# Kernel tuning notes

Measured on AMD Instinct MI355X. Metric: run time of the kernel, lower is better.

The kernel has to match this reference:

```python
import jax, jax.numpy as jnp
import numpy as np

N, B, FIN, FOUT = 4096, 16, 128, 128
DENSITY = 0.01


def setup_inputs() -> dict:
    key = jax.random.key(0)
    k1, k2, k3, k4 = jax.random.split(key, 4)
    # sparse binary adjacency (static pattern), stored dense for the reference
    adj = (jax.random.uniform(k1, (N, N)) < DENSITY).astype(jnp.float32)
    x = jax.random.normal(k2, (B, N, FIN), dtype=jnp.float32)
    W = jax.random.normal(k3, (FOUT, FIN), dtype=jnp.float32) * (1.0 / np.sqrt(FIN))
    b = jax.random.normal(k4, (FOUT,), dtype=jnp.float32) * 0.01
    return {"adj": adj, "x": x, "W": W, "b": b}


def _normalized_adj(adj):
    # A_hat = D^{-1/2} (A + I) D^{-1/2}, degrees from column sums (dim=0 in torch)
    a_self = adj + jnp.eye(adj.shape[0], dtype=adj.dtype)
    dinv = jax.lax.rsqrt(jnp.sum(a_self, axis=0))
    return dinv[:, None] * a_self * dinv[None, :]


def reference(adj, x, W, b):
    a_norm = _normalized_adj(adj)
    # SpMM aggregation over nodes: (N,N) x (B,N,F) -> (B,N,F)
    agg = jnp.einsum('nm,bmf->bnf', a_norm, x)
    # dense linear transform: fc(agg)
    return jnp.einsum('bnf,of->bno', agg, W) + b
```

## Files before the change

kernel.cpp:

```cpp
#include <hip/hip_runtime.h>


#define NN 4096
#define FD 128
#define NB 16
#define CAP 96
#define CPAD 104
#define XB 512

typedef float     f32x4 __attribute__((ext_vector_type(4)));
typedef _Float16  f16x4 __attribute__((ext_vector_type(4)));
typedef _Float16  f16x8 __attribute__((ext_vector_type(8)));
typedef int       i32x2 __attribute__((ext_vector_type(2)));

#define XP 136

__global__ __launch_bounds__(256) void k_bx(const float* __restrict__ A,
                                            float* __restrict__ deg,
                                            int* __restrict__ cnt,
                                            unsigned short* __restrict__ csr,
                                            const float* __restrict__ x,
                                            const float* __restrict__ W,
                                            _Float16* __restrict__ y) {
    __shared__ __align__(16) char smem[FD * XP * 2];
    const int t = threadIdx.x;

    if (blockIdx.x < XB) {
        _Float16 (*sW)[XP] = (_Float16(*)[XP])smem;
        const size_t rbase = (size_t)blockIdx.x * 128;

        #pragma unroll
        for (int i = 0; i < 8; ++i) {
            const int id = t + i * 256;
            const int o = id >> 4, f8 = (id & 15) * 8;
            const f32x4 a = *(const f32x4*)&W[(size_t)o * FD + f8];
            const f32x4 b = *(const f32x4*)&W[(size_t)o * FD + f8 + 4];
            f16x8 h;
            h[0]=(_Float16)a.x; h[1]=(_Float16)a.y; h[2]=(_Float16)a.z; h[3]=(_Float16)a.w;
            h[4]=(_Float16)b.x; h[5]=(_Float16)b.y; h[6]=(_Float16)b.z; h[7]=(_Float16)b.w;
            *(f16x8*)&sW[o][f8] = h;
        }
        __syncthreads();

        const int w = t >> 6, lane = t & 63;
        const int lrow = lane & 15, koct = (lane >> 4) * 8;
        const float* xr0 = x + (rbase + w * 32 + lrow) * FD;
        const float* xr1 = xr0 + 16 * FD;
        f32x4 acc[2][8] = {};
        #pragma unroll
        for (int kc = 0; kc < 4; ++kc) {
            const int ko = kc * 32 + koct;
            const f32x4 a0 = *(const f32x4*)&xr0[ko];
            const f32x4 a1 = *(const f32x4*)&xr0[ko + 4];
            const f32x4 b0 = *(const f32x4*)&xr1[ko];
            const f32x4 b1 = *(const f32x4*)&xr1[ko + 4];
            f16x8 xx0, xx1;
            xx0[0]=(_Float16)a0.x; xx0[1]=(_Float16)a0.y; xx0[2]=(_Float16)a0.z; xx0[3]=(_Float16)a0.w;
            xx0[4]=(_Float16)a1.x; xx0[5]=(_Float16)a1.y; xx0[6]=(_Float16)a1.z; xx0[7]=(_Float16)a1.w;
            xx1[0]=(_Float16)b0.x; xx1[1]=(_Float16)b0.y; xx1[2]=(_Float16)b0.z; xx1[3]=(_Float16)b0.w;
            xx1[4]=(_Float16)b1.x; xx1[5]=(_Float16)b1.y; xx1[6]=(_Float16)b1.z; xx1[7]=(_Float16)b1.w;
            #pragma unroll
            for (int ot = 0; ot < 8; ++ot) {
                const f16x8 ww = *(const f16x8*)&sW[ot * 16 + lrow][ko];
                acc[0][ot] = __builtin_amdgcn_mfma_f32_16x16x32_f16(ww, xx0, acc[0][ot], 0, 0, 0);
                acc[1][ot] = __builtin_amdgcn_mfma_f32_16x16x32_f16(ww, xx1, acc[1][ot], 0, 0, 0);
            }
        }
        #pragma unroll
        for (int rt = 0; rt < 2; ++rt) {
            const size_t row = rbase + w * 32 + rt * 16 + (lane & 15);
            #pragma unroll
            for (int ot = 0; ot < 8; ++ot) {
                f16x4 h;
                h[0] = (_Float16)acc[rt][ot][0];
                h[1] = (_Float16)acc[rt][ot][1];
                h[2] = (_Float16)acc[rt][ot][2];
                h[3] = (_Float16)acc[rt][ot][3];
                *(f16x4*)&y[row * FD + ot * 16 + (lane >> 4) * 4] = h;
            }
        }
        return;
    }

    int* sCnt = (int*)smem;
    const int n = blockIdx.x - XB;
    const float* row = A + (size_t)n * NN + t * 16;
    float r[16];
    *(f32x4*)&r[0]  = ((const f32x4*)row)[0];
    *(f32x4*)&r[4]  = ((const f32x4*)row)[1];
    *(f32x4*)&r[8]  = ((const f32x4*)row)[2];
    *(f32x4*)&r[12] = ((const f32x4*)row)[3];

    int c = 0;
    #pragma unroll
    for (int j = 0; j < 16; ++j) c += (r[j] != 0.0f) ? 1 : 0;
    sCnt[t] = c;
    __syncthreads();
    for (int off = 1; off < 256; off <<= 1) {
        const int v = sCnt[t];
        const int u = (t >= off) ? sCnt[t - off] : 0;
        __syncthreads();
        sCnt[t] = v + u;
        __syncthreads();
    }
    int pos = sCnt[t] - c;
    #pragma unroll
    for (int j = 0; j < 16; ++j) {
        if (r[j] != 0.0f) {
            const int m = t * 16 + j;
            if (pos < CAP) csr[(size_t)n * CAP + pos] = (unsigned short)m;
            ++pos;
            atomicAdd(&deg[m], 1.0f);
        }
    }
    if (t == 255) {
        int tot = sCnt[255];
        cnt[n] = tot < CAP ? tot : CAP;
    }
}

__global__ __launch_bounds__(256) void k_agg2(const _Float16* __restrict__ y,
                                              const int* __restrict__ cnt,
                                              const unsigned short* __restrict__ csr,
                                              const float* __restrict__ deg,
                                              const float* __restrict__ bias,
                                              float* __restrict__ out) {
    __shared__ int sL[4][CPAD * 2];
    const int t = threadIdx.x, w = t >> 6, lane = t & 63;
    const int bid = blockIdx.x;
    const int xcd = bid & 7;
    const int b0  = 2 * xcd;
    const int n   = (bid >> 3) * 4 + w;
    const int c = cnt[n];
    const int totPad = (c + 1 + 3) & ~3;

    for (int k = lane; k < CPAD; k += 64) {
        int m; float wv;
        if (k < c)       { m = csr[(size_t)n * CAP + k]; wv = rsqrtf(1.0f + deg[m]); }
        else if (k == c) { m = n; wv = rsqrtf(1.0f + deg[n]); }
        else             { m = n; wv = 0.0f; }
        sL[w][2 * k]     = m << 8;
        sL[w][2 * k + 1] = __float_as_int(wv);
    }
    __syncthreads();

    const int rq = lane >> 4;
    const int fo = (lane & 15) * 16;
    const char* yb0 = (const char*)y + (size_t)b0 * (NN * FD * 2);
    const char* yb1 = yb0 + (size_t)(NN * FD * 2);

    float acc0[8] = {}, acc1[8] = {};
    i32x2 e = *(const i32x2*)&sL[w][2 * rq];
    unsigned voff = (unsigned)(e.x + fo);
    f16x8 pA = *(const f16x8*)(yb0 + voff);
    f16x8 pB = *(const f16x8*)(yb1 + voff);
    float wt = __int_as_float(e.y);
    for (int k = rq + 4; k < totPad; k += 4) {
        const i32x2 e2 = *(const i32x2*)&sL[w][2 * k];
        const unsigned v2 = (unsigned)(e2.x + fo);
        const f16x8 nA = *(const f16x8*)(yb0 + v2);
        const f16x8 nB = *(const f16x8*)(yb1 + v2);
        const float wt2 = __int_as_float(e2.y);
        #pragma unroll
        for (int j = 0; j < 8; ++j) {
            acc0[j] = fmaf(wt, (float)pA[j], acc0[j]);
            acc1[j] = fmaf(wt, (float)pB[j], acc1[j]);
        }
        pA = nA; pB = nB; wt = wt2;
    }
    #pragma unroll
    for (int j = 0; j < 8; ++j) {
        acc0[j] = fmaf(wt, (float)pA[j], acc0[j]);
        acc1[j] = fmaf(wt, (float)pB[j], acc1[j]);
    }

    #pragma unroll
    for (int j = 0; j < 8; ++j) {
        acc0[j] += __shfl_xor(acc0[j], 16);
        acc0[j] += __shfl_xor(acc0[j], 32);
        acc1[j] += __shfl_xor(acc1[j], 16);
        acc1[j] += __shfl_xor(acc1[j], 32);
    }

    if (lane < 32) {
        const float dn = rsqrtf(1.0f + deg[n]);
        const int h = lane >> 4;
        const int f0 = (lane & 15) * 8 + h * 4;
        const f32x4 bb = *(const f32x4*)(bias + f0);
        f32x4 o0, o1;
        o0.x = acc0[h * 4 + 0] * dn + bb.x;
        o0.y = acc0[h * 4 + 1] * dn + bb.y;
        o0.z = acc0[h * 4 + 2] * dn + bb.z;
        o0.w = acc0[h * 4 + 3] * dn + bb.w;
        o1.x = acc1[h * 4 + 0] * dn + bb.x;
        o1.y = acc1[h * 4 + 1] * dn + bb.y;
        o1.z = acc1[h * 4 + 2] * dn + bb.z;
        o1.w = acc1[h * 4 + 3] * dn + bb.w;
        f32x4* d0 = (f32x4*)(out + ((size_t)b0 * NN + n) * FD + f0);
        f32x4* d1 = (f32x4*)(out + ((size_t)(b0 + 1) * NN + n) * FD + f0);
        __builtin_nontemporal_store(o0, d0);
        __builtin_nontemporal_store(o1, d1);
    }
}

extern "C" void kernel_launch(void* const* d_in, const int* in_sizes, int n_in,
                              void* d_out, int out_size, void* d_ws, size_t ws_size,
                              hipStream_t stream) {
    const float* A    = (const float*)d_in[0];
    const float* x    = (const float*)d_in[1];
    const float* W    = (const float*)d_in[2];
    const float* bias = (const float*)d_in[3];
    float* out = (float*)d_out;

    float*          deg  = (float*)d_ws;
    int*            cnt  = (int*)((char*)d_ws + 2 * NN * 4);
    unsigned short* csr  = (unsigned short*)(cnt + NN);
    _Float16*       y    = (_Float16*)((char*)d_ws + (3 * NN * 4 + (size_t)NN * CAP * 2));

    hipMemsetAsync(deg, 0, NN * sizeof(float), stream);
    k_bx  <<<XB + NN, 256, 0, stream>>>(A, deg, cnt, csr, x, W, y);
    k_agg2<<<(NN / 4) * (NB / 2), 256, 0, stream>>>(y, cnt, csr, deg, bias, out);
}
```

Before: 75.92 us.

## Split fused build/transform kernel, use wave-shuffle scan and fma_mix accumulation

Splits the fused kernel back into a separate feature transform (64 rows per block, more blocks) and an adjacency CSR build, launched sequentially. The CSR build replaces the shared-memory block scan, which had many barriers, with a wave-level shuffle scan plus a small cross-wave sum. The aggregation loop uses inline v_fma_mix_f32 so half-precision values are multiplied and accumulated directly without separate conversions. Running the transform and the build as sequential launches gives up the overlap the fused kernel allowed and adds a launch.

```diff
diff --git a/kernel.cpp b/kernel.cpp
--- a/kernel.cpp
+++ b/kernel.cpp
@@ -6,84 +6,83 @@
 #define NB 16
 #define CAP 96
 #define CPAD 104
-#define XB 512
 
 typedef float     f32x4 __attribute__((ext_vector_type(4)));
 typedef _Float16  f16x4 __attribute__((ext_vector_type(4)));
 typedef _Float16  f16x8 __attribute__((ext_vector_type(8)));
 typedef int       i32x2 __attribute__((ext_vector_type(2)));
+typedef int       i32x4 __attribute__((ext_vector_type(4)));
 
 #define XP 136
 
-__global__ __launch_bounds__(256) void k_bx(const float* __restrict__ A,
-                                            float* __restrict__ deg,
-                                            int* __restrict__ cnt,
-                                            unsigned short* __restrict__ csr,
-                                            const float* __restrict__ x,
-                                            const float* __restrict__ W,
-                                            _Float16* __restrict__ y) {
-    __shared__ __align__(16) char smem[FD * XP * 2];
+__device__ __forceinline__ float fmamix_lo(float acc, int pk, float w) {
+    asm("v_fma_mix_f32 %0, %1, %2, %0 op_sel:[0,0,0] op_sel_hi:[1,0,0]"
+        : "+v"(acc) : "v"(pk), "v"(w));
+    return acc;
+}
+__device__ __forceinline__ float fmamix_hi(float acc, int pk, float w) {
+    asm("v_fma_mix_f32 %0, %1, %2, %0 op_sel:[1,0,0] op_sel_hi:[1,0,0]"
+        : "+v"(acc) : "v"(pk), "v"(w));
+    return acc;
+}
+
+__global__ __launch_bounds__(256) void k_xform(const float* __restrict__ x,
+                                               const float* __restrict__ W,
+                                               _Float16* __restrict__ y) {
+    __shared__ _Float16 sW[FD][XP];
     const int t = threadIdx.x;
 
-    if (blockIdx.x < XB) {
-        _Float16 (*sW)[XP] = (_Float16(*)[XP])smem;
-        const size_t rbase = (size_t)blockIdx.x * 128;
-
+    #pragma unroll
+    for (int i = 0; i < 8; ++i) {
+        const int id = t + i * 256;
+        const int o = id >> 4, f8 = (id & 15) * 8;
+        const f32x4 a = *(const f32x4*)&W[(size_t)o * FD + f8];
+        const f32x4 b = *(const f32x4*)&W[(size_t)o * FD + f8 + 4];
+        f16x8 h;
+        h[0]=(_Float16)a.x; h[1]=(_Float16)a.y; h[2]=(_Float16)a.z; h[3]=(_Float16)a.w;
+        h[4]=(_Float16)b.x; h[5]=(_Float16)b.y; h[6]=(_Float16)b.z; h[7]=(_Float16)b.w;
+        *(f16x8*)&sW[o][f8] = h;
+    }
+    __syncthreads();
+
+    const int w = t >> 6, lane = t & 63;
+    const int lrow = lane & 15, koct = (lane >> 4) * 8;
+    const size_t rbase = (size_t)blockIdx.x * 64;
+    const float* xr = x + (rbase + w * 16 + lrow) * FD;
+    f32x4 acc[8] = {};
+    #pragma unroll
+    for (int kc = 0; kc < 4; ++kc) {
+        const int ko = kc * 32 + koct;
+        const f32x4 a0 = *(const f32x4*)&xr[ko];
+        const f32x4 a1 = *(const f32x4*)&xr[ko + 4];
+        f16x8 xx;
+        xx[0]=(_Float16)a0.x; xx[1]=(_Float16)a0.y; xx[2]=(_Float16)a0.z; xx[3]=(_Float16)a0.w;
+        xx[4]=(_Float16)a1.x; xx[5]=(_Float16)a1.y; xx[6]=(_Float16)a1.z; xx[7]=(_Float16)a1.w;
         #pragma unroll
-        for (int i = 0; i < 8; ++i) {
-            const int id = t + i * 256;
-            const int o = id >> 4, f8 = (id & 15) * 8;
-            const f32x4 a = *(const f32x4*)&W[(size_t)o * FD + f8];
-            const f32x4 b = *(const f32x4*)&W[(size_t)o * FD + f8 + 4];
-            f16x8 h;
-            h[0]=(_Float16)a.x; h[1]=(_Float16)a.y; h[2]=(_Float16)a.z; h[3]=(_Float16)a.w;
-            h[4]=(_Float16)b.x; h[5]=(_Float16)b.y; h[6]=(_Float16)b.z; h[7]=(_Float16)b.w;
-            *(f16x8*)&sW[o][f8] = h;
+        for (int ot = 0; ot < 8; ++ot) {
+            const f16x8 ww = *(const f16x8*)&sW[ot * 16 + lrow][ko];
+            acc[ot] = __builtin_amdgcn_mfma_f32_16x16x32_f16(ww, xx, acc[ot], 0, 0, 0);
         }
-        __syncthreads();
-
-        const int w = t >> 6, lane = t & 63;
-        const int lrow = lane & 15, koct = (lane >> 4) * 8;
-        const float* xr0 = x + (rbase + w * 32 + lrow) * FD;
-        const float* xr1 = xr0 + 16 * FD;
-        f32x4 acc[2][8] = {};
-        #pragma unroll
-        for (int kc = 0; kc < 4; ++kc) {
-            const int ko = kc * 32 + koct;
-            const f32x4 a0 = *(const f32x4*)&xr0[ko];
-            const f32x4 a1 = *(const f32x4*)&xr0[ko + 4];
-            const f32x4 b0 = *(const f32x4*)&xr1[ko];
-            const f32x4 b1 = *(const f32x4*)&xr1[ko + 4];
-            f16x8 xx0, xx1;
-            xx0[0]=(_Float16)a0.x; xx0[1]=(_Float16)a0.y; xx0[2]=(_Float16)a0.z; xx0[3]=(_Float16)a0.w;
-            xx0[4]=(_Float16)a1.x; xx0[5]=(_Float16)a1.y; xx0[6]=(_Float16)a1.z; xx0[7]=(_Float16)a1.w;
-            xx1[0]=(_Float16)b0.x; xx1[1]=(_Float16)b0.y; xx1[2]=(_Float16)b0.z; xx1[3]=(_Float16)b0.w;
-            xx1[4]=(_Float16)b1.x; xx1[5]=(_Float16)b1.y; xx1[6]=(_Float16)b1.z; xx1[7]=(_Float16)b1.w;
-            #pragma unroll
-            for (int ot = 0; ot < 8; ++ot) {
-                const f16x8 ww = *(const f16x8*)&sW[ot * 16 + lrow][ko];
-                acc[0][ot] = __builtin_amdgcn_mfma_f32_16x16x32_f16(ww, xx0, acc[0][ot], 0, 0, 0);
-                acc[1][ot] = __builtin_amdgcn_mfma_f32_16x16x32_f16(ww, xx1, acc[1][ot], 0, 0, 0);
-            }
-        }
-        #pragma unroll
-        for (int rt = 0; rt < 2; ++rt) {
-            const size_t row = rbase + w * 32 + rt * 16 + (lane & 15);
-            #pragma unroll
-            for (int ot = 0; ot < 8; ++ot) {
-                f16x4 h;
-                h[0] = (_Float16)acc[rt][ot][0];
-                h[1] = (_Float16)acc[rt][ot][1];
-                h[2] = (_Float16)acc[rt][ot][2];
-                h[3] = (_Float16)acc[rt][ot][3];
-                *(f16x4*)&y[row * FD + ot * 16 + (lane >> 4) * 4] = h;
-            }
-        }
-        return;
-    }
-
-    int* sCnt = (int*)smem;
-    const int n = blockIdx.x - XB;
+    }
+    const size_t row = rbase + w * 16 + (lane & 15);
+    #pragma unroll
+    for (int ot = 0; ot < 8; ++ot) {
+        f16x4 h;
+        h[0] = (_Float16)acc[ot][0];
+        h[1] = (_Float16)acc[ot][1];
+        h[2] = (_Float16)acc[ot][2];
+        h[3] = (_Float16)acc[ot][3];
+        *(f16x4*)&y[row * FD + ot * 16 + (lane >> 4) * 4] = h;
+    }
+}
+
+__global__ __launch_bounds__(256) void k_build(const float* __restrict__ A,
+                                               float* __restrict__ deg,
+                                               int* __restrict__ cnt,
+                                               unsigned short* __restrict__ csr) {
+    __shared__ int sWsum[4];
+    const int n = blockIdx.x, t = threadIdx.x;
+    const int w = t >> 6, lane = t & 63;
     const float* row = A + (size_t)n * NN + t * 16;
     float r[16];
     *(f32x4*)&r[0]  = ((const f32x4*)row)[0];
@@ -94,16 +93,20 @@
     int c = 0;
     #pragma unroll
     for (int j = 0; j < 16; ++j) c += (r[j] != 0.0f) ? 1 : 0;
-    sCnt[t] = c;
+
+    int s = c;
+    #pragma unroll
+    for (int off = 1; off < 64; off <<= 1) {
+        const int u = __shfl(s, lane - off);
+        s += (lane >= off) ? u : 0;
+    }
+    if (lane == 63) sWsum[w] = s;
     __syncthreads();
-    for (int off = 1; off < 256; off <<= 1) {
-        const int v = sCnt[t];
-        const int u = (t >= off) ? sCnt[t - off] : 0;
-        __syncthreads();
-        sCnt[t] = v + u;
-        __syncthreads();
-    }
-    int pos = sCnt[t] - c;
+    int wbase = 0;
+    #pragma unroll
+    for (int j = 0; j < 4; ++j) wbase += (j < w) ? sWsum[j] : 0;
+
+    int pos = wbase + s - c;
     #pragma unroll
     for (int j = 0; j < 16; ++j) {
         if (r[j] != 0.0f) {
@@ -114,7 +117,7 @@
         }
     }
     if (t == 255) {
-        int tot = sCnt[255];
+        const int tot = wbase + s;
         cnt[n] = tot < CAP ? tot : CAP;
     }
 }
@@ -152,26 +155,30 @@
     float acc0[8] = {}, acc1[8] = {};
     i32x2 e = *(const i32x2*)&sL[w][2 * rq];
     unsigned voff = (unsigned)(e.x + fo);
-    f16x8 pA = *(const f16x8*)(yb0 + voff);
-    f16x8 pB = *(const f16x8*)(yb1 + voff);
+    i32x4 pA = *(const i32x4*)(yb0 + voff);
+    i32x4 pB = *(const i32x4*)(yb1 + voff);
     float wt = __int_as_float(e.y);
     for (int k = rq + 4; k < totPad; k += 4) {
         const i32x2 e2 = *(const i32x2*)&sL[w][2 * k];
         const unsigned v2 = (unsigned)(e2.x + fo);
-        const f16x8 nA = *(const f16x8*)(yb0 + v2);
-        const f16x8 nB = *(const f16x8*)(yb1 + v2);
+        const i32x4 nA = *(const i32x4*)(yb0 + v2);
+        const i32x4 nB = *(const i32x4*)(yb1 + v2);
         const float wt2 = __int_as_float(e2.y);
         #pragma unroll
-        for (int j = 0; j < 8; ++j) {
-            acc0[j] = fmaf(wt, (float)pA[j], acc0[j]);
-            acc1[j] = fmaf(wt, (float)pB[j], acc1[j]);
+        for (int j = 0; j < 4; ++j) {
+            acc0[2*j]   = fmamix_lo(acc0[2*j],   pA[j], wt);
+            acc0[2*j+1] = fmamix_hi(acc0[2*j+1], pA[j], wt);
+            acc1[2*j]   = fmamix_lo(acc1[2*j],   pB[j], wt);
+            acc1[2*j+1] = fmamix_hi(acc1[2*j+1], pB[j], wt);
         }
         pA = nA; pB = nB; wt = wt2;
     }
     #pragma unroll
-    for (int j = 0; j < 8; ++j) {
-        acc0[j] = fmaf(wt, (float)pA[j], acc0[j]);
-        acc1[j] = fmaf(wt, (float)pB[j], acc1[j]);
+    for (int j = 0; j < 4; ++j) {
+        acc0[2*j]   = fmamix_lo(acc0[2*j],   pA[j], wt);
+        acc0[2*j+1] = fmamix_hi(acc0[2*j+1], pA[j], wt);
+        acc1[2*j]   = fmamix_lo(acc1[2*j],   pB[j], wt);
+        acc1[2*j+1] = fmamix_hi(acc1[2*j+1], pB[j], wt);
     }
 
     #pragma unroll
@@ -218,6 +225,7 @@
     _Float16*       y    = (_Float16*)((char*)d_ws + (3 * NN * 4 + (size_t)NN * CAP * 2));
 
     hipMemsetAsync(deg, 0, NN * sizeof(float), stream);
-    k_bx  <<<XB + NN, 256, 0, stream>>>(A, deg, cnt, csr, x, W, y);
-    k_agg2<<<(NN / 4) * (NB / 2), 256, 0, stream>>>(y, cnt, csr, deg, bias, out);
-}
+    k_xform<<<(NB * NN) / 64, 256, 0, stream>>>(x, W, y);
+    k_build<<<NN, 256, 0, stream>>>(A, deg, cnt, csr);
+    k_agg2 <<<(NN / 4) * (NB / 2), 256, 0, stream>>>(y, cnt, csr, deg, bias, out);
+}
```

After: 81.29 us. 1.07x slower.
